# Optimization experiments

Hardware: AMD Instinct MI355X
Metric: run time of the kernel (lower is better)

The kernel has to match this reference:

```python
import jax, jax.numpy as jnp
import numpy as np

PI = 3.141592653589793
N = 4194304


def _lerp(a, b, w):
    return a + w * (b - a)


def _schlick(u):
    m = jnp.clip(1.0 - u, 0.0, 1.0)
    return m ** 5


def setup_inputs() -> dict:
    key = jax.random.key(0)
    kl, kv, kp = jax.random.split(key, 3)

    def unit_dirs(k):
        v = jax.random.normal(k, (N, 3), dtype=jnp.float32)
        v = v / jnp.linalg.norm(v, axis=-1, keepdims=True)
        # upper hemisphere so most samples pass the cos_nl/cos_nv >= 0 test
        return v.at[:, 2].set(jnp.abs(v[:, 2]))

    light = unit_dirs(kl)
    view = unit_dirs(kv)
    inputs = jnp.stack([light, view], axis=1)  # [N, 2, 3]

    return {
        "inputs": inputs,
        "base_color": jnp.array([0.8, 0.8, 0.8], dtype=jnp.float32),
        "metallic": jnp.array([0.3], dtype=jnp.float32),
        "subsurface": jnp.array([0.2], dtype=jnp.float32),
        "specular": jnp.array([0.5], dtype=jnp.float32),
        "roughness": jnp.array([0.5], dtype=jnp.float32),
        "specular_tint": jnp.array([0.1], dtype=jnp.float32),
        "anisotropic": jnp.array([0.2], dtype=jnp.float32),
        "sheen": jnp.array([0.3], dtype=jnp.float32),
        "sheen_tint": jnp.array([0.5], dtype=jnp.float32),
        "clear_coat": jnp.array([0.5], dtype=jnp.float32),
        "clear_coat_gloss": jnp.array([0.8], dtype=jnp.float32),
    }


def _brdf(inputs, base_color, metallic, subsurface, specular, roughness,
          specular_tint, anisotropic, sheen, sheen_tint, clear_coat,
          clear_coat_gloss):
    # scalar params
    mtl = metallic[0]; sub = subsurface[0]; spec = specular[0]
    rough = roughness[0]; sp_tint = specular_tint[0]; aniso = anisotropic[0]
    sh = sheen[0]; sh_tint = sheen_tint[0]; cc = clear_coat[0]
    cc_gloss = clear_coat_gloss[0]

    light = inputs[:, 0, :]  # [N, 3]
    view = inputs[:, 1, :]   # [N, 3]
    hv = light + view
    half = hv / jnp.linalg.norm(hv, axis=-1, keepdims=True)

    # tangent x=[1,0,0], bitangent y=[0,1,0], normal=[0,0,1]
    cos_nl = light[:, 2]
    cos_nv = view[:, 2]
    cos_nh = half[:, 2]
    cos_hl = jnp.sum(half * light, axis=-1)

    valid = (cos_nl >= 0) & (cos_nv >= 0)
    # grad-safe cosines for invalid (masked-out) samples
    cnl = jnp.where(valid, cos_nl, 0.5)
    cnv = jnp.where(valid, cos_nv, 0.5)

    cd_lin = base_color ** 2.2  # mon2lin
    cd_lum = 0.3 * cd_lin[0] + 0.6 * cd_lin[1] + 0.1 * cd_lin[2]
    c_tint = jnp.where(cd_lum > 0, cd_lin / jnp.maximum(cd_lum, 1e-20),
                       jnp.zeros(3, cd_lin.dtype))

    c_spec0 = _lerp(spec * 0.08 * _lerp(1.0, c_tint, sp_tint), cd_lin, mtl)  # [3]
    c_sheen = _lerp(1.0, c_tint, sh_tint)  # [3]

    fl = _schlick(cnl)
    fv = _schlick(cnv)
    fd90 = 0.5 + 2.0 * cos_hl ** 2 * rough
    fd = _lerp(1.0, fd90, fl) * _lerp(1.0, fd90, fv)
    fss90 = cos_hl ** 2 * rough
    fss = _lerp(1.0, fss90, fl) * _lerp(1.0, fss90, fv)
    ss = 1.25 * (fss * (1.0 / (cnl + cnv) - 0.5) + 0.5)

    aspect = jnp.sqrt(1.0 - aniso * 0.9)
    ax = jnp.maximum(0.001, rough ** 2 / aspect)
    ay = jnp.maximum(0.001, rough ** 2 * aspect)

    # GTR2 anisotropic distribution
    Ds = 1.0 / (PI * ax * ay * ((half[:, 0] / ax) ** 2 +
                                (half[:, 1] / ay) ** 2 + cos_nh ** 2) ** 2)
    FH = _schlick(cos_hl)
    Fs = _lerp(c_spec0[None, :], 1.0, FH[:, None])  # [N, 3]

    def g_aniso(c, cx, cy):
        return 1.0 / (c + jnp.sqrt((cx * ax) ** 2 + (cy * ay) ** 2 + c ** 2))

    Gs = g_aniso(cnl, light[:, 0], light[:, 1]) * g_aniso(cnv, view[:, 0], view[:, 1])
    specular_term = (Gs * Ds)[:, None] * Fs

    Fsheen = FH[:, None] * sh * c_sheen[None, :]
    diffuse = ((1.0 / PI) * _lerp(fd, ss, sub)[:, None] * cd_lin[None, :] +
               Fsheen) * (1.0 - mtl)

    # clearcoat: GTR1 with a = lerp(0.1, 0.001, gloss)
    a_cc = _lerp(0.1, 0.001, cc_gloss)
    a2 = a_cc ** 2
    t = 1.0 + (a2 - 1.0) * cos_nh ** 2
    Dr = jnp.where(a_cc >= 1.0, 1.0 / PI, (a2 - 1.0) / (PI * jnp.log(a2) * t))

    def g025(c):
        a = 0.0625  # 0.25^2
        return 1.0 / (c + jnp.sqrt(a + c ** 2 - a * c ** 2))

    Gr = g025(cnl) * g025(cnv)
    Fr = _lerp(0.04, 1.0, FH)
    clear = 0.25 * cc * Gr * Fr * Dr

    out = diffuse + specular_term + clear[:, None]
    return jnp.where(valid[:, None], out, 0.0)


@jax.jit
def reference(inputs, base_color, metallic, subsurface, specular, roughness,
              specular_tint, anisotropic, sheen, sheen_tint, clear_coat,
              clear_coat_gloss):
    return _brdf(inputs, base_color, metallic, subsurface, specular, roughness,
                 specular_tint, anisotropic, sheen, sheen_tint, clear_coat,
                 clear_coat_gloss)
```

## Files before the change

kernel.cpp:

```cpp
#include <hip/hip_runtime.h>

#define PI_F 3.14159265358979323846f

__device__ __forceinline__ float rcpf_(float x){ return __builtin_amdgcn_rcpf(x); }
__device__ __forceinline__ float rsqf_(float x){ return __builtin_amdgcn_rsqf(x); }
__device__ __forceinline__ float sqrtf_(float x){ return __builtin_amdgcn_sqrtf(x); }

__device__ __forceinline__ float schlick5(float u){
    float m = fminf(fmaxf(1.0f - u, 0.0f), 1.0f);
    float m2 = m * m;
    return m2 * m2 * m;
}

__global__ __launch_bounds__(256) void brdf_kernel(
    const float* __restrict__ in,
    const float* __restrict__ base_color,
    const float* __restrict__ metallic,
    const float* __restrict__ subsurface,
    const float* __restrict__ specular,
    const float* __restrict__ roughness,
    const float* __restrict__ specular_tint,
    const float* __restrict__ anisotropic,
    const float* __restrict__ sheen,
    const float* __restrict__ sheen_tint,
    const float* __restrict__ clear_coat,
    const float* __restrict__ clear_coat_gloss,
    float* __restrict__ out,
    int npts)
{
    const float mtl     = metallic[0];
    const float sub     = subsurface[0];
    const float spec    = specular[0];
    const float rough   = roughness[0];
    const float sp_tint = specular_tint[0];
    const float aniso   = anisotropic[0];
    const float sh      = sheen[0];
    const float sh_tint = sheen_tint[0];
    const float cc      = clear_coat[0];
    const float ccg     = clear_coat_gloss[0];

    const float cd0 = __powf(base_color[0], 2.2f);
    const float cd1 = __powf(base_color[1], 2.2f);
    const float cd2 = __powf(base_color[2], 2.2f);
    const float lum = 0.3f*cd0 + 0.6f*cd1 + 0.1f*cd2;
    const float il  = rcpf_(fmaxf(lum, 1e-20f));
    const float ct0 = (lum > 0.f) ? cd0*il : 0.f;
    const float ct1 = (lum > 0.f) ? cd1*il : 0.f;
    const float ct2 = (lum > 0.f) ? cd2*il : 0.f;

    const float s008 = spec * 0.08f;
    const float b0 = s008 * (1.f + sp_tint*(ct0 - 1.f));
    const float b1 = s008 * (1.f + sp_tint*(ct1 - 1.f));
    const float b2 = s008 * (1.f + sp_tint*(ct2 - 1.f));
    const float cs0_0 = b0 + mtl*(cd0 - b0);
    const float cs0_1 = b1 + mtl*(cd1 - b1);
    const float cs0_2 = b2 + mtl*(cd2 - b2);

    const float om = 1.f - mtl;
    const float invpi = 1.f / PI_F;
    const float dcol0 = cd0 * om * invpi;
    const float dcol1 = cd1 * om * invpi;
    const float dcol2 = cd2 * om * invpi;
    const float scol0 = sh * (1.f + sh_tint*(ct0 - 1.f)) * om;
    const float scol1 = sh * (1.f + sh_tint*(ct1 - 1.f)) * om;
    const float scol2 = sh * (1.f + sh_tint*(ct2 - 1.f)) * om;

    const float two_rough = 2.f * rough;

    const float aspect = sqrtf_(1.f - aniso*0.9f);
    const float r2 = rough * rough;
    const float ax = fmaxf(0.001f, r2 * rcpf_(aspect));
    const float ay = fmaxf(0.001f, r2 * aspect);
    const float ax2 = ax*ax, ay2 = ay*ay;
    const float inv_ax2 = rcpf_(ax2);
    const float inv_ay2 = rcpf_(ay2);
    const float k_ds = rcpf_(PI_F * ax * ay);

    const float a_cc = 0.1f + (0.001f - 0.1f)*ccg;
    const float a2 = a_cc * a_cc;
    float a2m1, k_dr;
    if (a_cc >= 1.0f) { a2m1 = 0.f; k_dr = invpi; }
    else              { a2m1 = a2 - 1.f; k_dr = (a2 - 1.f) * rcpf_(PI_F * __logf(a2)); }
    const float cc_q = 0.25f * cc;

    int t = blockIdx.x * blockDim.x + threadIdx.x;
    long base = (long)t * 4;
    if (base >= npts) return;

    const float4* in4 = reinterpret_cast<const float4*>(in) + (size_t)t * 6;
    float4 q0 = in4[0], q1 = in4[1], q2 = in4[2], q3 = in4[3], q4 = in4[4], q5 = in4[5];

    const float px[4][6] = {
        {q0.x, q0.y, q0.z, q0.w, q1.x, q1.y},
        {q1.z, q1.w, q2.x, q2.y, q2.z, q2.w},
        {q3.x, q3.y, q3.z, q3.w, q4.x, q4.y},
        {q4.z, q4.w, q5.x, q5.y, q5.z, q5.w},
    };
    float ox[4][3];

#pragma unroll
    for (int k = 0; k < 4; ++k) {
        const float l0 = px[k][0], l1 = px[k][1], l2 = px[k][2];
        const float v0 = px[k][3], v1 = px[k][4], v2 = px[k][5];

        float hx = l0 + v0, hy = l1 + v1, hz = l2 + v2;
        const float inv = rsqf_(hx*hx + hy*hy + hz*hz);
        hx *= inv; hy *= inv; hz *= inv;

        const float cnh = hz;
        const float chl = hx*l0 + hy*l1 + hz*l2;

        const bool valid = (l2 >= 0.f) && (v2 >= 0.f);
        const float cnl = valid ? l2 : 0.5f;
        const float cnv = valid ? v2 : 0.5f;

        const float fl = schlick5(cnl);
        const float fv = schlick5(cnv);
        const float FH = schlick5(chl);

        const float chl2 = chl * chl;
        const float fd90m1  = two_rough * chl2 - 0.5f;
        const float fd  = (1.f + fd90m1*fl) * (1.f + fd90m1*fv);
        const float fss90m1 = rough * chl2 - 1.f;
        const float fss = (1.f + fss90m1*fl) * (1.f + fss90m1*fv);
        const float ss = 1.25f * (fss * (rcpf_(cnl + cnv) - 0.5f) + 0.5f);
        const float dw = fd + sub * (ss - fd);

        const float dterm = hx*hx*inv_ax2 + hy*hy*inv_ay2 + cnh*cnh;
        const float Ds = k_ds * rcpf_(dterm * dterm);
        const float GsL = rcpf_(cnl + sqrtf_(l0*l0*ax2 + l1*l1*ay2 + cnl*cnl));
        const float GsV = rcpf_(cnv + sqrtf_(v0*v0*ax2 + v1*v1*ay2 + cnv*cnv));
        const float GsDs = GsL * GsV * Ds;

        const float tcc = 1.f + a2m1 * cnh * cnh;
        const float Dr = k_dr * rcpf_(tcc);
        const float GrL = rcpf_(cnl + sqrtf_(0.0625f + 0.9375f*cnl*cnl));
        const float GrV = rcpf_(cnv + sqrtf_(0.0625f + 0.9375f*cnv*cnv));
        const float Fr = 0.04f + 0.96f * FH;
        const float clear = cc_q * GrL * GrV * Fr * Dr;

        float o0 = dw*dcol0 + FH*scol0 + GsDs*(cs0_0 + FH*(1.f - cs0_0)) + clear;
        float o1 = dw*dcol1 + FH*scol1 + GsDs*(cs0_1 + FH*(1.f - cs0_1)) + clear;
        float o2 = dw*dcol2 + FH*scol2 + GsDs*(cs0_2 + FH*(1.f - cs0_2)) + clear;

        ox[k][0] = valid ? o0 : 0.f;
        ox[k][1] = valid ? o1 : 0.f;
        ox[k][2] = valid ? o2 : 0.f;
    }

    float4* out4 = reinterpret_cast<float4*>(out) + (size_t)t * 3;
    out4[0] = make_float4(ox[0][0], ox[0][1], ox[0][2], ox[1][0]);
    out4[1] = make_float4(ox[1][1], ox[1][2], ox[2][0], ox[2][1]);
    out4[2] = make_float4(ox[2][2], ox[3][0], ox[3][1], ox[3][2]);
}

extern "C" void kernel_launch(void* const* d_in, const int* in_sizes, int n_in,
                              void* d_out, int out_size, void* d_ws, size_t ws_size,
                              hipStream_t stream) {
    const float* in = (const float*)d_in[0];
    const int npts = in_sizes[0] / 6;
    const int nthreads = npts / 4;
    const int block = 256;
    const int grid = (nthreads + block - 1) / block;

    brdf_kernel<<<grid, block, 0, stream>>>(
        in,
        (const float*)d_in[1],
        (const float*)d_in[2],
        (const float*)d_in[3],
        (const float*)d_in[4],
        (const float*)d_in[5],
        (const float*)d_in[6],
        (const float*)d_in[7],
        (const float*)d_in[8],
        (const float*)d_in[9],
        (const float*)d_in[10],
        (const float*)d_in[11],
        (float*)d_out, npts);
}
```

Before: 189.3 us.

## Precompute BRDF uniforms in a setup kernel and simplify half-vector algebra

Adds a single-thread setup kernel that computes the 22 material-derived constants into workspace, so the main kernel loads them instead of recomputing them per thread. The main kernel no longer normalizes the half vector. It uses cos_hl = 0.5*|l+v| for unit inputs and folds the normalization into the D and clearcoat denominators, merging several reciprocals into one. The clamp is dropped from the Schlick term. This relies on the inputs being unit vectors, adds a second launch per call, and may shift numerics slightly.

```diff
diff --git a/kernel.cpp b/kernel.cpp
--- a/kernel.cpp
+++ b/kernel.cpp
@@ -3,45 +3,22 @@
 #define PI_F 3.14159265358979323846f
 
 __device__ __forceinline__ float rcpf_(float x){ return __builtin_amdgcn_rcpf(x); }
-__device__ __forceinline__ float rsqf_(float x){ return __builtin_amdgcn_rsqf(x); }
 __device__ __forceinline__ float sqrtf_(float x){ return __builtin_amdgcn_sqrtf(x); }
 
 __device__ __forceinline__ float schlick5(float u){
-    float m = fminf(fmaxf(1.0f - u, 0.0f), 1.0f);
+    float m = 1.0f - u;
     float m2 = m * m;
     return m2 * m2 * m;
 }
 
-__global__ __launch_bounds__(256) void brdf_kernel(
-    const float* __restrict__ in,
-    const float* __restrict__ base_color,
-    const float* __restrict__ metallic,
-    const float* __restrict__ subsurface,
-    const float* __restrict__ specular,
-    const float* __restrict__ roughness,
-    const float* __restrict__ specular_tint,
-    const float* __restrict__ anisotropic,
-    const float* __restrict__ sheen,
-    const float* __restrict__ sheen_tint,
-    const float* __restrict__ clear_coat,
-    const float* __restrict__ clear_coat_gloss,
-    float* __restrict__ out,
-    int npts)
+__device__ __forceinline__ void compute_uniforms(
+    const float* bc, float mtl, float sub, float spec, float rough,
+    float sp_tint, float aniso, float sh, float sh_tint, float cc, float ccg,
+    float* u)
 {
-    const float mtl     = metallic[0];
-    const float sub     = subsurface[0];
-    const float spec    = specular[0];
-    const float rough   = roughness[0];
-    const float sp_tint = specular_tint[0];
-    const float aniso   = anisotropic[0];
-    const float sh      = sheen[0];
-    const float sh_tint = sheen_tint[0];
-    const float cc      = clear_coat[0];
-    const float ccg     = clear_coat_gloss[0];
-
-    const float cd0 = __powf(base_color[0], 2.2f);
-    const float cd1 = __powf(base_color[1], 2.2f);
-    const float cd2 = __powf(base_color[2], 2.2f);
+    const float cd0 = __powf(bc[0], 2.2f);
+    const float cd1 = __powf(bc[1], 2.2f);
+    const float cd2 = __powf(bc[2], 2.2f);
     const float lum = 0.3f*cd0 + 0.6f*cd1 + 0.1f*cd2;
     const float il  = rcpf_(fmaxf(lum, 1e-20f));
     const float ct0 = (lum > 0.f) ? cd0*il : 0.f;
@@ -58,34 +35,91 @@
 
     const float om = 1.f - mtl;
     const float invpi = 1.f / PI_F;
-    const float dcol0 = cd0 * om * invpi;
-    const float dcol1 = cd1 * om * invpi;
-    const float dcol2 = cd2 * om * invpi;
-    const float scol0 = sh * (1.f + sh_tint*(ct0 - 1.f)) * om;
-    const float scol1 = sh * (1.f + sh_tint*(ct1 - 1.f)) * om;
-    const float scol2 = sh * (1.f + sh_tint*(ct2 - 1.f)) * om;
-
-    const float two_rough = 2.f * rough;
 
     const float aspect = sqrtf_(1.f - aniso*0.9f);
     const float r2 = rough * rough;
     const float ax = fmaxf(0.001f, r2 * rcpf_(aspect));
     const float ay = fmaxf(0.001f, r2 * aspect);
-    const float ax2 = ax*ax, ay2 = ay*ay;
-    const float inv_ax2 = rcpf_(ax2);
-    const float inv_ay2 = rcpf_(ay2);
-    const float k_ds = rcpf_(PI_F * ax * ay);
 
     const float a_cc = 0.1f + (0.001f - 0.1f)*ccg;
     const float a2 = a_cc * a_cc;
     float a2m1, k_dr;
     if (a_cc >= 1.0f) { a2m1 = 0.f; k_dr = invpi; }
     else              { a2m1 = a2 - 1.f; k_dr = (a2 - 1.f) * rcpf_(PI_F * __logf(a2)); }
-    const float cc_q = 0.25f * cc;
+
+    u[0] = rough;
+    u[1] = sub;
+    u[2] = ax*ax;
+    u[3] = ay*ay;
+    u[4] = rcpf_(ax*ax);
+    u[5] = rcpf_(ay*ay);
+    u[6] = rcpf_(PI_F * ax * ay);
+    u[7] = a2m1;
+    u[8] = k_dr;
+    u[9] = 0.25f * cc;
+    u[10] = cd0 * om * invpi;
+    u[11] = cd1 * om * invpi;
+    u[12] = cd2 * om * invpi;
+    u[13] = sh * (1.f + sh_tint*(ct0 - 1.f)) * om;
+    u[14] = sh * (1.f + sh_tint*(ct1 - 1.f)) * om;
+    u[15] = sh * (1.f + sh_tint*(ct2 - 1.f)) * om;
+    u[16] = cs0_0;
+    u[17] = cs0_1;
+    u[18] = cs0_2;
+    u[19] = 1.f - cs0_0;
+    u[20] = 1.f - cs0_1;
+    u[21] = 1.f - cs0_2;
+}
+
+__global__ void setup_kernel(
+    const float* __restrict__ bc, const float* __restrict__ metallic,
+    const float* __restrict__ subsurface, const float* __restrict__ specular,
+    const float* __restrict__ roughness, const float* __restrict__ specular_tint,
+    const float* __restrict__ anisotropic, const float* __restrict__ sheen,
+    const float* __restrict__ sheen_tint, const float* __restrict__ clear_coat,
+    const float* __restrict__ clear_coat_gloss, float* __restrict__ ws)
+{
+    if (threadIdx.x == 0) {
+        float u[22];
+        compute_uniforms(bc, metallic[0], subsurface[0], specular[0], roughness[0],
+                         specular_tint[0], anisotropic[0], sheen[0], sheen_tint[0],
+                         clear_coat[0], clear_coat_gloss[0], u);
+        #pragma unroll
+        for (int i = 0; i < 22; ++i) ws[i] = u[i];
+    }
+}
+
+template<bool USE_WS>
+__global__ __launch_bounds__(256) void brdf_kernel(
+    const float* __restrict__ in,
+    const float* __restrict__ uws,
+    const float* __restrict__ bc, const float* __restrict__ metallic,
+    const float* __restrict__ subsurface, const float* __restrict__ specular,
+    const float* __restrict__ roughness, const float* __restrict__ specular_tint,
+    const float* __restrict__ anisotropic, const float* __restrict__ sheen,
+    const float* __restrict__ sheen_tint, const float* __restrict__ clear_coat,
+    const float* __restrict__ clear_coat_gloss,
+    float* __restrict__ out,
+    int npts)
+{
+    float U[22];
+    if constexpr (USE_WS) {
+        #pragma unroll
+        for (int i = 0; i < 22; ++i) U[i] = uws[i];
+    } else {
+        compute_uniforms(bc, metallic[0], subsurface[0], specular[0], roughness[0],
+                         specular_tint[0], anisotropic[0], sheen[0], sheen_tint[0],
+                         clear_coat[0], clear_coat_gloss[0], U);
+    }
+    const float rough   = U[0],  sub     = U[1];
+    const float ax2     = U[2],  ay2     = U[3];
+    const float inv_ax2 = U[4],  inv_ay2 = U[5];
+    const float k_ds    = U[6],  a2m1    = U[7];
+    const float k_dr    = U[8],  cc_q    = U[9];
+    const float two_rough = 2.f * rough;
 
     int t = blockIdx.x * blockDim.x + threadIdx.x;
-    long base = (long)t * 4;
-    if (base >= npts) return;
+    if ((long)t * 4 >= npts) return;
 
     const float4* in4 = reinterpret_cast<const float4*>(in) + (size_t)t * 6;
     float4 q0 = in4[0], q1 = in4[1], q2 = in4[2], q3 = in4[3], q4 = in4[4], q5 = in4[5];
@@ -103,12 +137,10 @@
         const float l0 = px[k][0], l1 = px[k][1], l2 = px[k][2];
         const float v0 = px[k][3], v1 = px[k][4], v2 = px[k][5];
 
-        float hx = l0 + v0, hy = l1 + v1, hz = l2 + v2;
-        const float inv = rsqf_(hx*hx + hy*hy + hz*hz);
-        hx *= inv; hy *= inv; hz *= inv;
-
-        const float cnh = hz;
-        const float chl = hx*l0 + hy*l1 + hz*l2;
+        const float hvx = l0 + v0, hvy = l1 + v1, hvz = l2 + v2;
+        const float n2 = hvx*hvx + hvy*hvy + hvz*hvz;
+        const float chl = 0.5f * sqrtf_(n2);
+        const float chl2 = 0.25f * n2;
 
         const bool valid = (l2 >= 0.f) && (v2 >= 0.f);
         const float cnl = valid ? l2 : 0.5f;
@@ -118,7 +150,6 @@
         const float fv = schlick5(cnv);
         const float FH = schlick5(chl);
 
-        const float chl2 = chl * chl;
         const float fd90m1  = two_rough * chl2 - 0.5f;
         const float fd  = (1.f + fd90m1*fl) * (1.f + fd90m1*fv);
         const float fss90m1 = rough * chl2 - 1.f;
@@ -126,22 +157,21 @@
         const float ss = 1.25f * (fss * (rcpf_(cnl + cnv) - 0.5f) + 0.5f);
         const float dw = fd + sub * (ss - fd);
 
-        const float dterm = hx*hx*inv_ax2 + hy*hy*inv_ay2 + cnh*cnh;
-        const float Ds = k_ds * rcpf_(dterm * dterm);
-        const float GsL = rcpf_(cnl + sqrtf_(l0*l0*ax2 + l1*l1*ay2 + cnl*cnl));
-        const float GsV = rcpf_(cnv + sqrtf_(v0*v0*ax2 + v1*v1*ay2 + cnv*cnv));
-        const float GsDs = GsL * GsV * Ds;
-
-        const float tcc = 1.f + a2m1 * cnh * cnh;
-        const float Dr = k_dr * rcpf_(tcc);
-        const float GrL = rcpf_(cnl + sqrtf_(0.0625f + 0.9375f*cnl*cnl));
-        const float GrV = rcpf_(cnv + sqrtf_(0.0625f + 0.9375f*cnv*cnv));
+        const float dtermu = hvx*hvx*inv_ax2 + hvy*hvy*inv_ay2 + hvz*hvz;
+        const float denL = cnl + sqrtf_(l0*l0*ax2 + l1*l1*ay2 + cnl*cnl);
+        const float denV = cnv + sqrtf_(v0*v0*ax2 + v1*v1*ay2 + cnv*cnv);
+        const float n2_2 = n2 * n2;
+        const float GsDs = k_ds * n2_2 * rcpf_(dtermu*dtermu * denL * denV);
+
+        const float tden = n2 + a2m1 * (hvz*hvz);
+        const float grL = cnl + sqrtf_(0.0625f + 0.9375f*cnl*cnl);
+        const float grV = cnv + sqrtf_(0.0625f + 0.9375f*cnv*cnv);
         const float Fr = 0.04f + 0.96f * FH;
-        const float clear = cc_q * GrL * GrV * Fr * Dr;
-
-        float o0 = dw*dcol0 + FH*scol0 + GsDs*(cs0_0 + FH*(1.f - cs0_0)) + clear;
-        float o1 = dw*dcol1 + FH*scol1 + GsDs*(cs0_1 + FH*(1.f - cs0_1)) + clear;
-        float o2 = dw*dcol2 + FH*scol2 + GsDs*(cs0_2 + FH*(1.f - cs0_2)) + clear;
+        const float clear = cc_q * Fr * k_dr * n2 * rcpf_(tden * grL * grV);
+
+        float o0 = dw*U[10] + FH*U[13] + GsDs*(U[16] + FH*U[19]) + clear;
+        float o1 = dw*U[11] + FH*U[14] + GsDs*(U[17] + FH*U[20]) + clear;
+        float o2 = dw*U[12] + FH*U[15] + GsDs*(U[18] + FH*U[21]) + clear;
 
         ox[k][0] = valid ? o0 : 0.f;
         ox[k][1] = valid ? o1 : 0.f;
@@ -163,18 +193,27 @@
     const int block = 256;
     const int grid = (nthreads + block - 1) / block;
 
-    brdf_kernel<<<grid, block, 0, stream>>>(
-        in,
-        (const float*)d_in[1],
-        (const float*)d_in[2],
-        (const float*)d_in[3],
-        (const float*)d_in[4],
-        (const float*)d_in[5],
-        (const float*)d_in[6],
-        (const float*)d_in[7],
-        (const float*)d_in[8],
-        (const float*)d_in[9],
-        (const float*)d_in[10],
-        (const float*)d_in[11],
-        (float*)d_out, npts);
-}
+    const float* bc  = (const float*)d_in[1];
+    const float* p2  = (const float*)d_in[2];
+    const float* p3  = (const float*)d_in[3];
+    const float* p4  = (const float*)d_in[4];
+    const float* p5  = (const float*)d_in[5];
+    const float* p6  = (const float*)d_in[6];
+    const float* p7  = (const float*)d_in[7];
+    const float* p8  = (const float*)d_in[8];
+    const float* p9  = (const float*)d_in[9];
+    const float* p10 = (const float*)d_in[10];
+    const float* p11 = (const float*)d_in[11];
+
+    if (ws_size >= 22 * sizeof(float) && d_ws != nullptr) {
+        float* ws = (float*)d_ws;
+        setup_kernel<<<1, 64, 0, stream>>>(bc, p2, p3, p4, p5, p6, p7, p8, p9, p10, p11, ws);
+        brdf_kernel<true><<<grid, block, 0, stream>>>(
+            in, ws, bc, p2, p3, p4, p5, p6, p7, p8, p9, p10, p11,
+            (float*)d_out, npts);
+    } else {
+        brdf_kernel<false><<<grid, block, 0, stream>>>(
+            in, nullptr, bc, p2, p3, p4, p5, p6, p7, p8, p9, p10, p11,
+            (float*)d_out, npts);
+    }
+}
```

Result: no change. 187.3 us (-1.1%).
